# Kernel tuning notes

Hardware: AMD Instinct MI355X
Metric: run time of the kernel (lower is better)

## Reference

```python
import jax, jax.numpy as jnp
import numpy as np

N_TOKENS = 4096
HIDDEN = 1024
FFN = 2048
N_EXPERTS = 8
TOP_K = 2


def setup_inputs() -> dict:
    key = jax.random.key(0)
    k1, k2, k3, k4 = jax.random.split(key, 4)
    x = jax.random.normal(k1, (N_TOKENS, HIDDEN), dtype=jnp.float32)
    router_weight = jax.random.normal(k2, (HIDDEN, N_EXPERTS), dtype=jnp.float32)
    # matches torch.randn(...) * 0.02 init scale
    w1 = jax.random.normal(k3, (HIDDEN, FFN * N_EXPERTS), dtype=jnp.float32) * 0.02
    w2 = jax.random.normal(k4, (FFN * N_EXPERTS, HIDDEN), dtype=jnp.float32) * 0.02
    return {"x": x, "router_weight": router_weight, "w1": w1, "w2": w2, "top_k": TOP_K}


def reference(x, router_weight, w1, w2, top_k):
    # x: [N, H]; router_weight: [H, E]; w1: [H, E*F]; w2: [E*F, H]
    N, H = x.shape
    E = router_weight.shape[1]
    F = w1.shape[1] // E

    # --- routing (router in fp32, softmax over experts, top-k probs) ---
    logits = x.astype(jnp.float32) @ router_weight            # [N, E]
    probs = jax.nn.softmax(logits, axis=-1)                   # [N, E]
    topk_probs, topk_idx = jax.lax.top_k(probs, top_k)        # [N, k]

    # --- expert FFN: per-expert gelu(x @ w1_e) @ w2_e ---
    # Dense formulation: compute every expert for every token, then gather the
    # top-k outputs per token. Same math as grouped-GEMM dispatch/combine.
    h = jax.nn.gelu(x @ w1, approximate=False)                # [N, E*F]
    h = h.reshape(N, E, F)
    w2e = w2.reshape(E, F, H)
    y = jnp.einsum('nef,efh->neh', h, w2e)                    # [N, E, H]

    # --- combine: weight selected expert outputs by router probs, sum top-k ---
    sel = jnp.take_along_axis(y, topk_idx[:, :, None], axis=1)   # [N, k, H]
    out = (sel * topk_probs[:, :, None].astype(sel.dtype)).sum(axis=1)  # [N, H]
    return out
```

## Files before the change

### kernel.cpp

```cpp
#include <hip/hip_runtime.h>
#include <hip/hip_bf16.h>
#include <math.h>

#define N_TOK 4096
#define HID   1024
#define FFN   2048
#define NEXP  8
#define WROW  (NEXP*FFN)
#define NSLOT (N_TOK*2)
#define NCHUNK (NSLOT/64)

typedef __attribute__((ext_vector_type(4))) float f32x4;
typedef __attribute__((ext_vector_type(8))) short short8;

__device__ inline unsigned short f2bf(float f) {
  union { float f; unsigned u; } v; v.f = f;
  unsigned r = v.u + 0x7fffu + ((v.u >> 16) & 1u);
  return (unsigned short)(r >> 16);
}
__device__ __forceinline__ float bf2f(unsigned short u) {
  union { unsigned u; float f; } v; v.u = ((unsigned)u) << 16; return v.f;
}

__device__ __forceinline__ float gelu_f(float v) {
  const float u = 1.5957691216057308f * v + 0.07135481627f * (v * v * v);
  return v / (1.f + __expf(-u));
}

__device__ __forceinline__ void gload16(const void* g, void* l) {
  __builtin_amdgcn_global_load_lds((const __attribute__((address_space(1))) void*)g,
                                   (__attribute__((address_space(3))) void*)l, 16, 0, 0);
}


__global__ __launch_bounds__(256) void router_kernel(
    const float* __restrict__ x, const float* __restrict__ rw,
    int* __restrict__ eidx, float* __restrict__ probs,
    unsigned short* __restrict__ xb) {
  __shared__ float rwT[NEXP][HID];
  const int t = threadIdx.x;
  #pragma unroll
  for (int it = 0; it < 8; ++it) {
    const int flat = t * 4 + it * 1024;
    const f32x4 v = *(const f32x4*)&rw[flat];
    #pragma unroll
    for (int j = 0; j < 4; ++j) rwT[(flat + j) & 7][(flat + j) >> 3] = v[j];
  }
  __syncthreads();

  const int w = t >> 6, l = t & 63;
  const int n = blockIdx.x * 4 + w;
  const float* xr = x + (size_t)n * HID;
  float acc[NEXP];
  #pragma unroll
  for (int e = 0; e < NEXP; ++e) acc[e] = 0.f;

  #pragma unroll
  for (int j = 0; j < 4; ++j) {
    const int i = l * 4 + j * 256;
    const f32x4 xv = *(const f32x4*)&xr[i];
    if (xb) {
      ushort4 o;
      o.x = f2bf(xv[0]); o.y = f2bf(xv[1]); o.z = f2bf(xv[2]); o.w = f2bf(xv[3]);
      *(ushort4*)&xb[(size_t)n * HID + i] = o;
    }
    #pragma unroll
    for (int e = 0; e < NEXP; ++e) {
      const f32x4 wv = *(const f32x4*)&rwT[e][i];
      acc[e] += xv[0] * wv[0] + xv[1] * wv[1] + xv[2] * wv[2] + xv[3] * wv[3];
    }
  }
  #pragma unroll
  for (int e = 0; e < NEXP; ++e) {
    float s = acc[e];
    #pragma unroll
    for (int off = 32; off; off >>= 1) s += __shfl_xor(s, off);
    acc[e] = s;
  }
  if (l == 0) {
    float m = acc[0];
    #pragma unroll
    for (int e = 1; e < NEXP; ++e) m = fmaxf(m, acc[e]);
    float p[NEXP]; float den = 0.f;
    #pragma unroll
    for (int e = 0; e < NEXP; ++e) { p[e] = expf(acc[e] - m); den += p[e]; }
    const float inv = 1.f / den;
    int e1 = 0; float b1 = -1.f;
    #pragma unroll
    for (int e = 0; e < NEXP; ++e) if (p[e] > b1) { b1 = p[e]; e1 = e; }
    int e2 = 0; float b2 = -1.f;
    #pragma unroll
    for (int e = 0; e < NEXP; ++e) if (e != e1 && p[e] > b2) { b2 = p[e]; e2 = e; }
    eidx[n * 2 + 0] = e1; eidx[n * 2 + 1] = e2;
    probs[n * 2 + 0] = b1 * inv; probs[n * 2 + 1] = b2 * inv;
  }
}

__global__ __launch_bounds__(256) void dispatch_kernel(
    const int* __restrict__ eidx, const float* __restrict__ probs,
    int* __restrict__ counts, int* __restrict__ offs,
    int* __restrict__ rowtok, float* __restrict__ rowprob,
    int* __restrict__ tokslot) {
  __shared__ int chunkbase[NCHUNK][NEXP];
  __shared__ int tot[NEXP], off_s[NEXP];
  const int t = threadIdx.x;
  const int w = t >> 6, l = t & 63;

  for (int c = w; c < NCHUNK; c += 4) {
    const int e = eidx[c * 64 + l];
    #pragma unroll
    for (int xp = 0; xp < NEXP; ++xp) {
      const unsigned long long m = __ballot(e == xp);
      if (l == xp) chunkbase[c][xp] = __popcll(m);
    }
  }
  __syncthreads();

  if (t < NEXP) {
    int a = 0;
    for (int c = 0; c < NCHUNK; ++c) {
      const int v = chunkbase[c][t];
      chunkbase[c][t] = a;
      a += v;
    }
    tot[t] = a;
  }
  __syncthreads();
  if (t == 0) {
    int a = 0;
    for (int e = 0; e < NEXP; ++e) { off_s[e] = a; offs[e] = a; counts[e] = tot[e]; a += tot[e]; }
  }
  __syncthreads();

  for (int c = w; c < NCHUNK; c += 4) {
    const int s = c * 64 + l;
    const int e = eidx[s];
    unsigned long long mask_e = 0;
    #pragma unroll
    for (int xp = 0; xp < NEXP; ++xp) {
      const unsigned long long m = __ballot(e == xp);
      if (e == xp) mask_e = m;
    }
    const unsigned long long below = mask_e & ((1ull << l) - 1ull);
    const int pos = off_s[e] + chunkbase[c][e] + __popcll(below);
    rowtok[pos]  = s >> 1;
    rowprob[pos] = probs[s];
    tokslot[s]   = pos;
  }
}

__global__ __launch_bounds__(256) void tconv_kernel(
    const float* __restrict__ in, unsigned short* __restrict__ out,
    int R, int C, int RB) {
  __shared__ float tile[64][65];
  const int r0 = blockIdx.y * 64, c0 = blockIdx.x * 64;
  const int t = threadIdx.x;
  const int tr = t >> 4;
  const int tc4 = (t & 15) * 4;
  #pragma unroll
  for (int i = 0; i < 4; ++i) {
    const int r = tr + i * 16;
    const f32x4 v = *(const f32x4*)&in[(size_t)(r0 + r) * C + c0 + tc4];
    tile[r][tc4 + 0] = v[0]; tile[r][tc4 + 1] = v[1];
    tile[r][tc4 + 2] = v[2]; tile[r][tc4 + 3] = v[3];
  }
  __syncthreads();
  const int eb  = r0 / RB;
  const int rm0 = r0 % RB;
  #pragma unroll
  for (int i = 0; i < 4; ++i) {
    const int c = tr + i * 16;
    ushort4 o;
    o.x = f2bf(tile[tc4 + 0][c]); o.y = f2bf(tile[tc4 + 1][c]);
    o.z = f2bf(tile[tc4 + 2][c]); o.w = f2bf(tile[tc4 + 3][c]);
    const size_t oidx = (size_t)eb * C * RB + (size_t)(c0 + c) * RB + rm0 + tc4;
    *(ushort4*)&out[oidx] = o;
  }
}

__global__ __launch_bounds__(256) void gemm1_fast(
    const unsigned short* __restrict__ xb, const unsigned short* __restrict__ w1t,
    const int* __restrict__ rowtok, const int* __restrict__ counts,
    const int* __restrict__ offs, unsigned short* __restrict__ h1) {
  int wg = blockIdx.x;
  wg = (wg & 7) * (8192 / 8) + (wg >> 3);
  const int bx = wg & 15;
  const int by = (wg >> 4) & 63;
  const int e  = wg >> 10;

  const int cnt = counts[e];
  const int m0  = by * 128;
  if (m0 >= cnt) return;
  const int n0  = bx * 128;
  const int seg = offs[e];

  __shared__ alignas(16) unsigned short Al[3][128 * 32];
  __shared__ alignas(16) unsigned short Bl[3][128 * 32];

  const int t  = threadIdx.x;
  const int l  = t & 63;
  const int w  = t >> 6;
  const int wr = w >> 1, wc = w & 1;
  const int lr = l & 15, hi = l >> 4;

  const int rowS = t >> 2;
  const int kc   = (((t & 3) ^ ((t >> 3) & 3)) * 8);
  const int ra0 = m0 + rowS      < cnt ? m0 + rowS      : cnt - 1;
  const int ra1 = m0 + rowS + 64 < cnt ? m0 + rowS + 64 : cnt - 1;
  const unsigned short* aptr0 = xb + (size_t)rowtok[seg + ra0] * HID + kc;
  const unsigned short* aptr1 = xb + (size_t)rowtok[seg + ra1] * HID + kc;
  const unsigned short* bptr0 = w1t + ((size_t)e * FFN + n0 + rowS)      * HID + kc;
  const unsigned short* bptr1 = w1t + ((size_t)e * FFN + n0 + rowS + 64) * HID + kc;
  const int ldst = (t & 192) * 8;
  const int koff = (hi ^ ((lr >> 1) & 3)) * 8;

  f32x4 acc[4][4];
  #pragma unroll
  for (int i = 0; i < 4; ++i)
    #pragma unroll
    for (int j = 0; j < 4; ++j) acc[i][j] = (f32x4){0.f, 0.f, 0.f, 0.f};

  auto STAGE = [&](int b, int k0) {
    gload16(aptr0 + k0, &Al[b][ldst]);
    gload16(aptr1 + k0, &Al[b][ldst + 2048]);
    gload16(bptr0 + k0, &Bl[b][ldst]);
    gload16(bptr1 + k0, &Bl[b][ldst + 2048]);
  };
  auto COMPUTE = [&](int b) {
    short8 af[4], bfr[4];
    #pragma unroll
    for (int mi = 0; mi < 4; ++mi) af[mi]  = *(const short8*)&Al[b][(wr * 64 + mi * 16 + lr) * 32 + koff];
    #pragma unroll
    for (int ni = 0; ni < 4; ++ni) bfr[ni] = *(const short8*)&Bl[b][(wc * 64 + ni * 16 + lr) * 32 + koff];
    __builtin_amdgcn_s_setprio(1);
    #pragma unroll
    for (int mi = 0; mi < 4; ++mi)
      #pragma unroll
      for (int ni = 0; ni < 4; ++ni)
        acc[mi][ni] = __builtin_amdgcn_mfma_f32_16x16x32_bf16(af[mi], bfr[ni], acc[mi][ni], 0, 0, 0);
    __builtin_amdgcn_s_setprio(0);
  };

  const int NT = HID / 32;
  STAGE(0, 0);
  STAGE(1, 32);
  asm volatile("s_waitcnt vmcnt(4)" ::: "memory");
  __builtin_amdgcn_s_barrier();
  __builtin_amdgcn_sched_barrier(0);
  int cur = 0;
  for (int tt = 0; tt < NT; ++tt) {
    if (tt + 2 < NT) {
      int b2 = cur + 2; if (b2 >= 3) b2 -= 3;
      STAGE(b2, (tt + 2) * 32);
    }
    COMPUTE(cur);
    if (tt + 1 < NT) {
      if (tt + 2 < NT) asm volatile("s_waitcnt vmcnt(4)" ::: "memory");
      else             asm volatile("s_waitcnt vmcnt(0)" ::: "memory");
      __builtin_amdgcn_s_barrier();
      __builtin_amdgcn_sched_barrier(0);
    }
    ++cur; if (cur == 3) cur = 0;
  }

  #pragma unroll
  for (int mi = 0; mi < 4; ++mi) {
    #pragma unroll
    for (int r = 0; r < 4; ++r) {
      const int grow = m0 + wr * 64 + mi * 16 + hi * 4 + r;
      if (grow < cnt) {
        const size_t rowoff = (size_t)(seg + grow) * FFN + n0 + wc * 64 + lr;
        #pragma unroll
        for (int ni = 0; ni < 4; ++ni)
          h1[rowoff + ni * 16] = f2bf(gelu_f(acc[mi][ni][r]));
      }
    }
  }
}

template<int KS>
__global__ __launch_bounds__(256) void gemm2_fast(
    const unsigned short* __restrict__ h1, const unsigned short* __restrict__ w2t,
    const int* __restrict__ counts, const int* __restrict__ offs,
    unsigned short* __restrict__ y) {
  constexpr int G = 8 * 64 * 8 * KS;
  int wg = blockIdx.x;
  wg = (wg & 7) * (G / 8) + (wg >> 3);
  const int bx  = wg & 7;
  const int by  = (wg >> 3) & 63;
  const int bzz = wg >> 9;
  const int e   = bzz & 7;
  const int kz  = bzz >> 3;

  const int cnt = counts[e];
  const int m0  = by * 128;
  if (m0 >= cnt) return;
  const int n0  = bx * 128;
  const int seg = offs[e];
  constexpr int KLEN = FFN / KS;
  const int kbase = kz * KLEN;

  __shared__ alignas(16) unsigned short Al[3][128 * 32];
  __shared__ alignas(16) unsigned short Bl[3][128 * 32];

  const int t  = threadIdx.x;
  const int l  = t & 63;
  const int w  = t >> 6;
  const int wr = w >> 1, wc = w & 1;
  const int lr = l & 15, hi = l >> 4;

  const int rowS = t >> 2;
  const int kc   = (((t & 3) ^ ((t >> 3) & 3)) * 8);
  const int ra0 = m0 + rowS      < cnt ? m0 + rowS      : cnt - 1;
  const int ra1 = m0 + rowS + 64 < cnt ? m0 + rowS + 64 : cnt - 1;
  const unsigned short* aptr0 = h1 + (size_t)(seg + ra0) * FFN + kbase + kc;
  const unsigned short* aptr1 = h1 + (size_t)(seg + ra1) * FFN + kbase + kc;
  const unsigned short* bptr0 = w2t + ((size_t)e * HID + n0 + rowS)      * FFN + kbase + kc;
  const unsigned short* bptr1 = w2t + ((size_t)e * HID + n0 + rowS + 64) * FFN + kbase + kc;
  const int ldst = (t & 192) * 8;
  const int koff = (hi ^ ((lr >> 1) & 3)) * 8;

  f32x4 acc[4][4];
  #pragma unroll
  for (int i = 0; i < 4; ++i)
    #pragma unroll
    for (int j = 0; j < 4; ++j) acc[i][j] = (f32x4){0.f, 0.f, 0.f, 0.f};

  auto STAGE = [&](int b, int k0) {
    gload16(aptr0 + k0, &Al[b][ldst]);
    gload16(aptr1 + k0, &Al[b][ldst + 2048]);
    gload16(bptr0 + k0, &Bl[b][ldst]);
    gload16(bptr1 + k0, &Bl[b][ldst + 2048]);
  };
  auto COMPUTE = [&](int b) {
    short8 af[4], bfr[4];
    #pragma unroll
    for (int mi = 0; mi < 4; ++mi) af[mi]  = *(const short8*)&Al[b][(wr * 64 + mi * 16 + lr) * 32 + koff];
    #pragma unroll
    for (int ni = 0; ni < 4; ++ni) bfr[ni] = *(const short8*)&Bl[b][(wc * 64 + ni * 16 + lr) * 32 + koff];
    __builtin_amdgcn_s_setprio(1);
    #pragma unroll
    for (int mi = 0; mi < 4; ++mi)
      #pragma unroll
      for (int ni = 0; ni < 4; ++ni)
        acc[mi][ni] = __builtin_amdgcn_mfma_f32_16x16x32_bf16(af[mi], bfr[ni], acc[mi][ni], 0, 0, 0);
    __builtin_amdgcn_s_setprio(0);
  };

  const int NT = KLEN / 32;
  STAGE(0, 0);
  STAGE(1, 32);
  asm volatile("s_waitcnt vmcnt(4)" ::: "memory");
  __builtin_amdgcn_s_barrier();
  __builtin_amdgcn_sched_barrier(0);
  int cur = 0;
  for (int tt = 0; tt < NT; ++tt) {
    if (tt + 2 < NT) {
      int b2 = cur + 2; if (b2 >= 3) b2 -= 3;
      STAGE(b2, (tt + 2) * 32);
    }
    COMPUTE(cur);
    if (tt + 1 < NT) {
      if (tt + 2 < NT) asm volatile("s_waitcnt vmcnt(4)" ::: "memory");
      else             asm volatile("s_waitcnt vmcnt(0)" ::: "memory");
      __builtin_amdgcn_s_barrier();
      __builtin_amdgcn_sched_barrier(0);
    }
    ++cur; if (cur == 3) cur = 0;
  }

  #pragma unroll
  for (int mi = 0; mi < 4; ++mi) {
    #pragma unroll
    for (int r = 0; r < 4; ++r) {
      const int grow = m0 + wr * 64 + mi * 16 + hi * 4 + r;
      if (grow < cnt) {
        const int slot = seg + grow;
        unsigned short* yrow = y + ((size_t)kz * NSLOT + slot) * HID + n0 + wc * 64 + lr;
        #pragma unroll
        for (int ni = 0; ni < 4; ++ni)
          yrow[ni * 16] = f2bf(acc[mi][ni][r]);
      }
    }
  }
}

template<int KS>
__global__ __launch_bounds__(256) void combine_kernel(
    const unsigned short* __restrict__ y, const int* __restrict__ tokslot,
    const float* __restrict__ probs, float* __restrict__ out) {
  const int n = blockIdx.x;
  const int c = threadIdx.x * 4;
  const int s1 = tokslot[n * 2 + 0], s2 = tokslot[n * 2 + 1];
  const float p1 = probs[n * 2 + 0], p2 = probs[n * 2 + 1];
  float r0 = 0.f, r1 = 0.f, r2 = 0.f, r3 = 0.f;
  #pragma unroll
  for (int kz = 0; kz < KS; ++kz) {
    const ushort4 a = *(const ushort4*)&y[((size_t)kz * NSLOT + s1) * HID + c];
    const ushort4 b = *(const ushort4*)&y[((size_t)kz * NSLOT + s2) * HID + c];
    r0 += p1 * bf2f(a.x) + p2 * bf2f(b.x);
    r1 += p1 * bf2f(a.y) + p2 * bf2f(b.y);
    r2 += p1 * bf2f(a.z) + p2 * bf2f(b.z);
    r3 += p1 * bf2f(a.w) + p2 * bf2f(b.w);
  }
  *(f32x4*)&out[(size_t)n * HID + c] = (f32x4){r0, r1, r2, r3};
}

__global__ __launch_bounds__(256) void gemm2_fast_atomic(
    const unsigned short* __restrict__ h1, const unsigned short* __restrict__ w2t,
    const int* __restrict__ rowtok, const float* __restrict__ rowprob,
    const int* __restrict__ counts, const int* __restrict__ offs,
    float* __restrict__ out) {
  const int e   = blockIdx.z;
  const int cnt = counts[e];
  const int m0  = blockIdx.y * 128;
  if (m0 >= cnt) return;
  const int n0  = blockIdx.x * 128;
  const int seg = offs[e];

  __shared__ alignas(16) unsigned short Al[128 * 32];
  __shared__ alignas(16) unsigned short Bl[128 * 32];

  const int t  = threadIdx.x;
  const int l  = t & 63;
  const int w  = t >> 6;
  const int wr = w >> 1, wc = w & 1;
  const int lr = l & 15, hi = l >> 4;

  const int rowS = t >> 2;
  const int kc   = (((t & 3) ^ ((t >> 3) & 3)) * 8);
  const int ra0 = m0 + rowS      < cnt ? m0 + rowS      : cnt - 1;
  const int ra1 = m0 + rowS + 64 < cnt ? m0 + rowS + 64 : cnt - 1;
  const unsigned short* aptr0 = h1 + (size_t)(seg + ra0) * FFN + kc;
  const unsigned short* aptr1 = h1 + (size_t)(seg + ra1) * FFN + kc;
  const unsigned short* bptr0 = w2t + ((size_t)e * HID + n0 + rowS)      * FFN + kc;
  const unsigned short* bptr1 = w2t + ((size_t)e * HID + n0 + rowS + 64) * FFN + kc;
  unsigned short* const ldsA0 = Al + (t & 192) * 8;
  unsigned short* const ldsB0 = Bl + (t & 192) * 8;
  const int koff = (hi ^ ((lr >> 1) & 3)) * 8;

  f32x4 acc[4][4];
  #pragma unroll
  for (int i = 0; i < 4; ++i)
    #pragma unroll
    for (int j = 0; j < 4; ++j) acc[i][j] = (f32x4){0.f, 0.f, 0.f, 0.f};

  for (int k0 = 0; k0 < FFN; k0 += 32) {
    gload16(aptr0 + k0, ldsA0);
    gload16(aptr1 + k0, ldsA0 + 2048);
    gload16(bptr0 + k0, ldsB0);
    gload16(bptr1 + k0, ldsB0 + 2048);
    __syncthreads();
    short8 af[4], bfr[4];
    #pragma unroll
    for (int mi = 0; mi < 4; ++mi) af[mi]  = *(const short8*)&Al[(wr * 64 + mi * 16 + lr) * 32 + koff];
    #pragma unroll
    for (int ni = 0; ni < 4; ++ni) bfr[ni] = *(const short8*)&Bl[(wc * 64 + ni * 16 + lr) * 32 + koff];
    #pragma unroll
    for (int mi = 0; mi < 4; ++mi)
      #pragma unroll
      for (int ni = 0; ni < 4; ++ni)
        acc[mi][ni] = __builtin_amdgcn_mfma_f32_16x16x32_bf16(af[mi], bfr[ni], acc[mi][ni], 0, 0, 0);
    __syncthreads();
  }

  #pragma unroll
  for (int mi = 0; mi < 4; ++mi) {
    #pragma unroll
    for (int r = 0; r < 4; ++r) {
      const int grow = m0 + wr * 64 + mi * 16 + hi * 4 + r;
      if (grow < cnt) {
        const int slot = seg + grow;
        const int tok  = rowtok[slot];
        const float p  = rowprob[slot];
        #pragma unroll
        for (int ni = 0; ni < 4; ++ni)
          atomicAdd(&out[(size_t)tok * HID + n0 + wc * 64 + ni * 16 + lr], p * acc[mi][ni][r]);
      }
    }
  }
}

__global__ __launch_bounds__(256) void gemm1_old(
    const float* __restrict__ x, const float* __restrict__ w1,
    const int* __restrict__ rowtok, const int* __restrict__ counts,
    const int* __restrict__ offs, unsigned short* __restrict__ h1) {
  const int e   = blockIdx.z;
  const int cnt = counts[e];
  const int m0  = blockIdx.y * 64;
  if (m0 >= cnt) return;
  const int n0  = blockIdx.x * 64;
  const int seg = offs[e];
  __shared__ unsigned short Al[64 * 40];
  __shared__ unsigned short Bl[64 * 40];
  const int t  = threadIdx.x;
  const int l  = t & 63;
  const int wv = t >> 6;
  const int wr = wv >> 1, wc = wv & 1;
  const int am  = t >> 2;
  const int akb = (t & 3) * 8;
  const int amg = m0 + am;
  const bool aval = (amg < cnt);
  const float* aptr = aval ? (x + (size_t)rowtok[seg + amg] * HID + akb) : x;
  const int bn  = t & 63;
  const int bkg = (t >> 6) * 8;
  const float* bptr = w1 + (size_t)e * FFN + n0 + bn;
  f32x4 acc[2][2];
  #pragma unroll
  for (int i = 0; i < 2; ++i)
    #pragma unroll
    for (int j = 0; j < 2; ++j) acc[i][j] = (f32x4){0.f, 0.f, 0.f, 0.f};
  const int kreg = (l >> 4) * 8;
  const int lr   = l & 15;
  for (int k0 = 0; k0 < HID; k0 += 32) {
    short8 av = (short8){0,0,0,0,0,0,0,0};
    if (aval) {
      const f32x4 v0 = *(const f32x4*)(aptr + k0);
      const f32x4 v1 = *(const f32x4*)(aptr + k0 + 4);
      #pragma unroll
      for (int j = 0; j < 4; ++j) { av[j] = (short)f2bf(v0[j]); av[4 + j] = (short)f2bf(v1[j]); }
    }
    *(short8*)&Al[am * 40 + akb] = av;
    short8 bv;
    #pragma unroll
    for (int j = 0; j < 8; ++j) bv[j] = (short)f2bf(bptr[(size_t)(k0 + bkg + j) * WROW]);
    *(short8*)&Bl[bn * 40 + bkg] = bv;
    __syncthreads();
    short8 af[2], bfr[2];
    #pragma unroll
    for (int mi = 0; mi < 2; ++mi) af[mi]  = *(const short8*)&Al[(wr * 32 + mi * 16 + lr) * 40 + kreg];
    #pragma unroll
    for (int ni = 0; ni < 2; ++ni) bfr[ni] = *(const short8*)&Bl[(wc * 32 + ni * 16 + lr) * 40 + kreg];
    #pragma unroll
    for (int mi = 0; mi < 2; ++mi)
      #pragma unroll
      for (int ni = 0; ni < 2; ++ni)
        acc[mi][ni] = __builtin_amdgcn_mfma_f32_16x16x32_bf16(af[mi], bfr[ni], acc[mi][ni], 0, 0, 0);
    __syncthreads();
  }
  const int kq = l >> 4;
  #pragma unroll
  for (int mi = 0; mi < 2; ++mi) {
    #pragma unroll
    for (int r = 0; r < 4; ++r) {
      const int grow = m0 + wr * 32 + mi * 16 + kq * 4 + r;
      if (grow < cnt) {
        #pragma unroll
        for (int ni = 0; ni < 2; ++ni) {
          const float v = acc[mi][ni][r];
          const float g = 0.5f * v * (1.0f + erff(v * 0.70710678118654752f));
          h1[(size_t)(seg + grow) * FFN + n0 + wc * 32 + ni * 16 + lr] = f2bf(g);
        }
      }
    }
  }
}

__global__ __launch_bounds__(256) void gemm2_old(
    const unsigned short* __restrict__ h1, const float* __restrict__ w2,
    const int* __restrict__ rowtok, const float* __restrict__ rowprob,
    const int* __restrict__ counts, const int* __restrict__ offs,
    float* __restrict__ out) {
  const int e   = blockIdx.z;
  const int cnt = counts[e];
  const int m0  = blockIdx.y * 64;
  if (m0 >= cnt) return;
  const int n0  = blockIdx.x * 64;
  const int seg = offs[e];
  __shared__ unsigned short Al[64 * 40];
  __shared__ unsigned short Bl[64 * 40];
  const int t  = threadIdx.x;
  const int l  = t & 63;
  const int wv = t >> 6;
  const int wr = wv >> 1, wc = wv & 1;
  const int am  = t >> 2;
  const int akb = (t & 3) * 8;
  const int amg = m0 + am;
  const bool aval = (amg < cnt);
  const unsigned short* aptr = aval ? (h1 + (size_t)(seg + amg) * FFN + akb) : h1;
  const int bn  = t & 63;
  const int bkg = (t >> 6) * 8;
  const float* bptr = w2 + (size_t)e * FFN * HID + n0 + bn;
  f32x4 acc[2][2];
  #pragma unroll
  for (int i = 0; i < 2; ++i)
    #pragma unroll
    for (int j = 0; j < 2; ++j) acc[i][j] = (f32x4){0.f, 0.f, 0.f, 0.f};
  const int kreg = (l >> 4) * 8;
  const int lr   = l & 15;
  for (int k0 = 0; k0 < FFN; k0 += 32) {
    short8 av = (short8){0,0,0,0,0,0,0,0};
    if (aval) av = *(const short8*)(aptr + k0);
    *(short8*)&Al[am * 40 + akb] = av;
    short8 bv;
    #pragma unroll
    for (int j = 0; j < 8; ++j) bv[j] = (short)f2bf(bptr[(size_t)(k0 + bkg + j) * HID]);
    *(short8*)&Bl[bn * 40 + bkg] = bv;
    __syncthreads();
    short8 af[2], bfr[2];
    #pragma unroll
    for (int mi = 0; mi < 2; ++mi) af[mi]  = *(const short8*)&Al[(wr * 32 + mi * 16 + lr) * 40 + kreg];
    #pragma unroll
    for (int ni = 0; ni < 2; ++ni) bfr[ni] = *(const short8*)&Bl[(wc * 32 + ni * 16 + lr) * 40 + kreg];
    #pragma unroll
    for (int mi = 0; mi < 2; ++mi)
      #pragma unroll
      for (int ni = 0; ni < 2; ++ni)
        acc[mi][ni] = __builtin_amdgcn_mfma_f32_16x16x32_bf16(af[mi], bfr[ni], acc[mi][ni], 0, 0, 0);
    __syncthreads();
  }
  const int kq = l >> 4;
  #pragma unroll
  for (int mi = 0; mi < 2; ++mi) {
    #pragma unroll
    for (int r = 0; r < 4; ++r) {
      const int grow = m0 + wr * 32 + mi * 16 + kq * 4 + r;
      if (grow < cnt) {
        const int slot = seg + grow;
        const int tok  = rowtok[slot];
        const float p  = rowprob[slot];
        #pragma unroll
        for (int ni = 0; ni < 2; ++ni)
          atomicAdd(&out[(size_t)tok * HID + n0 + wc * 32 + ni * 16 + lr], p * acc[mi][ni][r]);
      }
    }
  }
}

extern "C" void kernel_launch(void* const* d_in, const int* in_sizes, int n_in,
                              void* d_out, int out_size, void* d_ws, size_t ws_size,
                              hipStream_t stream) {
  const float* x  = (const float*)d_in[0];
  const float* rw = (const float*)d_in[1];
  const float* w1 = (const float*)d_in[2];
  const float* w2 = (const float*)d_in[3];
  float* out = (float*)d_out;

  int*   counts  = (int*)d_ws;
  int*   offs    = counts + 8;
  int*   tokslot = counts + 16;
  int*   eidx    = tokslot + NSLOT;
  float* probs   = (float*)(eidx + NSLOT);
  int*   rowtok  = (int*)(probs + NSLOT);
  float* rowprob = (float*)(rowtok + NSLOT);
  unsigned short* h1 = (unsigned short*)(rowprob + NSLOT);
  unsigned short* xb = h1 + (size_t)NSLOT * FFN;
  unsigned short* wt = xb + (size_t)N_TOK * HID;
  unsigned short* y  = wt + (size_t)WROW * HID;

  const size_t need_base = (size_t)((char*)y - (char*)d_ws);
  const size_t need_y1   = need_base + (size_t)NSLOT * HID * 2;
  const size_t need_y2   = need_base + (size_t)2 * NSLOT * HID * 2;
  const bool fast = (ws_size >= need_base);

  router_kernel<<<N_TOK / 4, 256, 0, stream>>>(x, rw, eidx, probs, fast ? xb : nullptr);
  dispatch_kernel<<<1, 256, 0, stream>>>(eidx, probs, counts, offs, rowtok, rowprob, tokslot);

  if (fast) {
    tconv_kernel<<<dim3(WROW / 64, HID / 64), 256, 0, stream>>>(w1, wt, HID, WROW, HID);
    gemm1_fast<<<16 * 64 * 8, 256, 0, stream>>>(xb, wt, rowtok, counts, offs, h1);
    tconv_kernel<<<dim3(HID / 64, WROW / 64), 256, 0, stream>>>(w2, wt, WROW, HID, FFN);
    if (ws_size >= need_y2) {
      gemm2_fast<2><<<8 * 64 * 8 * 2, 256, 0, stream>>>(h1, wt, counts, offs, y);
      combine_kernel<2><<<N_TOK, 256, 0, stream>>>(y, tokslot, probs, out);
    } else if (ws_size >= need_y1) {
      gemm2_fast<1><<<8 * 64 * 8, 256, 0, stream>>>(h1, wt, counts, offs, y);
      combine_kernel<1><<<N_TOK, 256, 0, stream>>>(y, tokslot, probs, out);
    } else {
      hipMemsetAsync(d_out, 0, (size_t)out_size * sizeof(float), stream);
      gemm2_fast_atomic<<<dim3(HID / 128, NSLOT / 128, NEXP), 256, 0, stream>>>(h1, wt, rowtok, rowprob, counts, offs, out);
    }
  } else {
    hipMemsetAsync(d_out, 0, (size_t)out_size * sizeof(float), stream);
    gemm1_old<<<dim3(FFN / 64, NSLOT / 64, NEXP), 256, 0, stream>>>(x, w1, rowtok, counts, offs, h1);
    gemm2_old<<<dim3(HID / 64, NSLOT / 64, NEXP), 256, 0, stream>>>(h1, w2, rowtok, rowprob, counts, offs, out);
  }
}
```

Baseline: 207.4 us.

## Shrink GEMM grids to persistent M-loop and merge weight conversions into one kernel

The grouped GEMMs now launch a fixed grid with nine M-tile slots per expert. Each block loops over M tiles with a stride of nine, instead of launching 64 M tiles per expert, most of which exit early. The two weight transpose-and-convert passes are merged into a single launch writing to separate buffers, which needs extra workspace. This removes early-exit blocks and a launch, but an expert with many tokens can leave some blocks running long serial loops.

```diff
diff --git a/kernel.cpp b/kernel.cpp
--- a/kernel.cpp
+++ b/kernel.cpp
@@ -178,19 +178,56 @@
   }
 }
 
+__global__ __launch_bounds__(256) void tconv_both_kernel(
+    const float* __restrict__ w1, const float* __restrict__ w2,
+    unsigned short* __restrict__ w1t, unsigned short* __restrict__ w2t) {
+  __shared__ float tile[64][65];
+  int b = blockIdx.x;
+  const float* in; unsigned short* out; int C, RB, r0, c0;
+  if (b < 4096) {
+    in = w1; out = w1t; C = WROW; RB = HID;
+    c0 = (b & 255) * 64; r0 = (b >> 8) * 64;
+  } else {
+    b -= 4096;
+    in = w2; out = w2t; C = HID; RB = FFN;
+    c0 = (b & 15) * 64; r0 = (b >> 4) * 64;
+  }
+  const int t = threadIdx.x;
+  const int tr = t >> 4;
+  const int tc4 = (t & 15) * 4;
+  #pragma unroll
+  for (int i = 0; i < 4; ++i) {
+    const int r = tr + i * 16;
+    const f32x4 v = *(const f32x4*)&in[(size_t)(r0 + r) * C + c0 + tc4];
+    tile[r][tc4 + 0] = v[0]; tile[r][tc4 + 1] = v[1];
+    tile[r][tc4 + 2] = v[2]; tile[r][tc4 + 3] = v[3];
+  }
+  __syncthreads();
+  const int eb  = r0 / RB;
+  const int rm0 = r0 % RB;
+  #pragma unroll
+  for (int i = 0; i < 4; ++i) {
+    const int c = tr + i * 16;
+    ushort4 o;
+    o.x = f2bf(tile[tc4 + 0][c]); o.y = f2bf(tile[tc4 + 1][c]);
+    o.z = f2bf(tile[tc4 + 2][c]); o.w = f2bf(tile[tc4 + 3][c]);
+    const size_t oidx = (size_t)eb * C * RB + (size_t)(c0 + c) * RB + rm0 + tc4;
+    *(ushort4*)&out[oidx] = o;
+  }
+}
+
 __global__ __launch_bounds__(256) void gemm1_fast(
     const unsigned short* __restrict__ xb, const unsigned short* __restrict__ w1t,
     const int* __restrict__ rowtok, const int* __restrict__ counts,
     const int* __restrict__ offs, unsigned short* __restrict__ h1) {
   int wg = blockIdx.x;
-  wg = (wg & 7) * (8192 / 8) + (wg >> 3);
+  wg = (wg & 7) * (1152 / 8) + (wg >> 3);
   const int bx = wg & 15;
-  const int by = (wg >> 4) & 63;
-  const int e  = wg >> 10;
+  const int rest = wg >> 4;
+  const int by = rest % 9;
+  const int e  = rest / 9;
 
   const int cnt = counts[e];
-  const int m0  = by * 128;
-  if (m0 >= cnt) return;
   const int n0  = bx * 128;
   const int seg = offs[e];
 
@@ -205,74 +242,81 @@
 
   const int rowS = t >> 2;
   const int kc   = (((t & 3) ^ ((t >> 3) & 3)) * 8);
-  const int ra0 = m0 + rowS      < cnt ? m0 + rowS      : cnt - 1;
-  const int ra1 = m0 + rowS + 64 < cnt ? m0 + rowS + 64 : cnt - 1;
-  const unsigned short* aptr0 = xb + (size_t)rowtok[seg + ra0] * HID + kc;
-  const unsigned short* aptr1 = xb + (size_t)rowtok[seg + ra1] * HID + kc;
-  const unsigned short* bptr0 = w1t + ((size_t)e * FFN + n0 + rowS)      * HID + kc;
-  const unsigned short* bptr1 = w1t + ((size_t)e * FFN + n0 + rowS + 64) * HID + kc;
+  const unsigned short* bptr0 = w1t + ((size_t)e * FFN + n0 + rowS) * HID + kc;
+  const unsigned short* bptr1 = bptr0 + (size_t)64 * HID;
   const int ldst = (t & 192) * 8;
   const int koff = (hi ^ ((lr >> 1) & 3)) * 8;
-
-  f32x4 acc[4][4];
-  #pragma unroll
-  for (int i = 0; i < 4; ++i)
-    #pragma unroll
-    for (int j = 0; j < 4; ++j) acc[i][j] = (f32x4){0.f, 0.f, 0.f, 0.f};
-
-  auto STAGE = [&](int b, int k0) {
-    gload16(aptr0 + k0, &Al[b][ldst]);
-    gload16(aptr1 + k0, &Al[b][ldst + 2048]);
-    gload16(bptr0 + k0, &Bl[b][ldst]);
-    gload16(bptr1 + k0, &Bl[b][ldst + 2048]);
-  };
-  auto COMPUTE = [&](int b) {
-    short8 af[4], bfr[4];
-    #pragma unroll
-    for (int mi = 0; mi < 4; ++mi) af[mi]  = *(const short8*)&Al[b][(wr * 64 + mi * 16 + lr) * 32 + koff];
-    #pragma unroll
-    for (int ni = 0; ni < 4; ++ni) bfr[ni] = *(const short8*)&Bl[b][(wc * 64 + ni * 16 + lr) * 32 + koff];
-    __builtin_amdgcn_s_setprio(1);
-    #pragma unroll
-    for (int mi = 0; mi < 4; ++mi)
-      #pragma unroll
-      for (int ni = 0; ni < 4; ++ni)
-        acc[mi][ni] = __builtin_amdgcn_mfma_f32_16x16x32_bf16(af[mi], bfr[ni], acc[mi][ni], 0, 0, 0);
-    __builtin_amdgcn_s_setprio(0);
-  };
-
   const int NT = HID / 32;
-  STAGE(0, 0);
-  STAGE(1, 32);
-  asm volatile("s_waitcnt vmcnt(4)" ::: "memory");
-  __builtin_amdgcn_s_barrier();
-  __builtin_amdgcn_sched_barrier(0);
-  int cur = 0;
-  for (int tt = 0; tt < NT; ++tt) {
-    if (tt + 2 < NT) {
-      int b2 = cur + 2; if (b2 >= 3) b2 -= 3;
-      STAGE(b2, (tt + 2) * 32);
-    }
-    COMPUTE(cur);
-    if (tt + 1 < NT) {
-      if (tt + 2 < NT) asm volatile("s_waitcnt vmcnt(4)" ::: "memory");
-      else             asm volatile("s_waitcnt vmcnt(0)" ::: "memory");
-      __builtin_amdgcn_s_barrier();
-      __builtin_amdgcn_sched_barrier(0);
-    }
-    ++cur; if (cur == 3) cur = 0;
-  }
-
-  #pragma unroll
-  for (int mi = 0; mi < 4; ++mi) {
-    #pragma unroll
-    for (int r = 0; r < 4; ++r) {
-      const int grow = m0 + wr * 64 + mi * 16 + hi * 4 + r;
-      if (grow < cnt) {
-        const size_t rowoff = (size_t)(seg + grow) * FFN + n0 + wc * 64 + lr;
+
+  bool firstm = true;
+  for (int m0 = by * 128; m0 < cnt; m0 += 9 * 128) {
+    if (!firstm) __syncthreads();
+    firstm = false;
+
+    const int ra0 = m0 + rowS      < cnt ? m0 + rowS      : cnt - 1;
+    const int ra1 = m0 + rowS + 64 < cnt ? m0 + rowS + 64 : cnt - 1;
+    const unsigned short* aptr0 = xb + (size_t)rowtok[seg + ra0] * HID + kc;
+    const unsigned short* aptr1 = xb + (size_t)rowtok[seg + ra1] * HID + kc;
+
+    f32x4 acc[4][4];
+    #pragma unroll
+    for (int i = 0; i < 4; ++i)
+      #pragma unroll
+      for (int j = 0; j < 4; ++j) acc[i][j] = (f32x4){0.f, 0.f, 0.f, 0.f};
+
+    auto STAGE = [&](int b, int k0) {
+      gload16(aptr0 + k0, &Al[b][ldst]);
+      gload16(aptr1 + k0, &Al[b][ldst + 2048]);
+      gload16(bptr0 + k0, &Bl[b][ldst]);
+      gload16(bptr1 + k0, &Bl[b][ldst + 2048]);
+    };
+    auto COMPUTE = [&](int b) {
+      short8 af[4], bfr[4];
+      #pragma unroll
+      for (int mi = 0; mi < 4; ++mi) af[mi]  = *(const short8*)&Al[b][(wr * 64 + mi * 16 + lr) * 32 + koff];
+      #pragma unroll
+      for (int ni = 0; ni < 4; ++ni) bfr[ni] = *(const short8*)&Bl[b][(wc * 64 + ni * 16 + lr) * 32 + koff];
+      __builtin_amdgcn_s_setprio(1);
+      #pragma unroll
+      for (int mi = 0; mi < 4; ++mi)
         #pragma unroll
         for (int ni = 0; ni < 4; ++ni)
-          h1[rowoff + ni * 16] = f2bf(gelu_f(acc[mi][ni][r]));
+          acc[mi][ni] = __builtin_amdgcn_mfma_f32_16x16x32_bf16(af[mi], bfr[ni], acc[mi][ni], 0, 0, 0);
+      __builtin_amdgcn_s_setprio(0);
+    };
+
+    STAGE(0, 0);
+    STAGE(1, 32);
+    asm volatile("s_waitcnt vmcnt(4)" ::: "memory");
+    __builtin_amdgcn_s_barrier();
+    __builtin_amdgcn_sched_barrier(0);
+    int cur = 0;
+    for (int tt = 0; tt < NT; ++tt) {
+      if (tt + 2 < NT) {
+        int b2 = cur + 2; if (b2 >= 3) b2 -= 3;
+        STAGE(b2, (tt + 2) * 32);
+      }
+      COMPUTE(cur);
+      if (tt + 1 < NT) {
+        if (tt + 2 < NT) asm volatile("s_waitcnt vmcnt(4)" ::: "memory");
+        else             asm volatile("s_waitcnt vmcnt(0)" ::: "memory");
+        __builtin_amdgcn_s_barrier();
+        __builtin_amdgcn_sched_barrier(0);
+      }
+      ++cur; if (cur == 3) cur = 0;
+    }
+
+    #pragma unroll
+    for (int mi = 0; mi < 4; ++mi) {
+      #pragma unroll
+      for (int r = 0; r < 4; ++r) {
+        const int grow = m0 + wr * 64 + mi * 16 + hi * 4 + r;
+        if (grow < cnt) {
+          const size_t rowoff = (size_t)(seg + grow) * FFN + n0 + wc * 64 + lr;
+          #pragma unroll
+          for (int ni = 0; ni < 4; ++ni)
+            h1[rowoff + ni * 16] = f2bf(gelu_f(acc[mi][ni][r]));
+        }
       }
     }
   }
@@ -283,18 +327,17 @@
     const unsigned short* __restrict__ h1, const unsigned short* __restrict__ w2t,
     const int* __restrict__ counts, const int* __restrict__ offs,
     unsigned short* __restrict__ y) {
-  constexpr int G = 8 * 64 * 8 * KS;
+  constexpr int G = 576 * KS;
   int wg = blockIdx.x;
   wg = (wg & 7) * (G / 8) + (wg >> 3);
   const int bx  = wg & 7;
-  const int by  = (wg >> 3) & 63;
-  const int bzz = wg >> 9;
-  const int e   = bzz & 7;
-  const int kz  = bzz >> 3;
+  int rest = wg >> 3;
+  const int by  = rest % 9;
+  rest /= 9;
+  const int e   = rest & 7;
+  const int kz  = rest >> 3;
 
   const int cnt = counts[e];
-  const int m0  = by * 128;
-  if (m0 >= cnt) return;
   const int n0  = bx * 128;
   const int seg = offs[e];
   constexpr int KLEN = FFN / KS;
@@ -311,75 +354,82 @@
 
   const int rowS = t >> 2;
   const int kc   = (((t & 3) ^ ((t >> 3) & 3)) * 8);
-  const int ra0 = m0 + rowS      < cnt ? m0 + rowS      : cnt - 1;
-  const int ra1 = m0 + rowS + 64 < cnt ? m0 + rowS + 64 : cnt - 1;
-  const unsigned short* aptr0 = h1 + (size_t)(seg + ra0) * FFN + kbase + kc;
-  const unsigned short* aptr1 = h1 + (size_t)(seg + ra1) * FFN + kbase + kc;
-  const unsigned short* bptr0 = w2t + ((size_t)e * HID + n0 + rowS)      * FFN + kbase + kc;
-  const unsigned short* bptr1 = w2t + ((size_t)e * HID + n0 + rowS + 64) * FFN + kbase + kc;
+  const unsigned short* bptr0 = w2t + ((size_t)e * HID + n0 + rowS) * FFN + kbase + kc;
+  const unsigned short* bptr1 = bptr0 + (size_t)64 * FFN;
   const int ldst = (t & 192) * 8;
   const int koff = (hi ^ ((lr >> 1) & 3)) * 8;
-
-  f32x4 acc[4][4];
-  #pragma unroll
-  for (int i = 0; i < 4; ++i)
-    #pragma unroll
-    for (int j = 0; j < 4; ++j) acc[i][j] = (f32x4){0.f, 0.f, 0.f, 0.f};
-
-  auto STAGE = [&](int b, int k0) {
-    gload16(aptr0 + k0, &Al[b][ldst]);
-    gload16(aptr1 + k0, &Al[b][ldst + 2048]);
-    gload16(bptr0 + k0, &Bl[b][ldst]);
-    gload16(bptr1 + k0, &Bl[b][ldst + 2048]);
-  };
-  auto COMPUTE = [&](int b) {
-    short8 af[4], bfr[4];
-    #pragma unroll
-    for (int mi = 0; mi < 4; ++mi) af[mi]  = *(const short8*)&Al[b][(wr * 64 + mi * 16 + lr) * 32 + koff];
-    #pragma unroll
-    for (int ni = 0; ni < 4; ++ni) bfr[ni] = *(const short8*)&Bl[b][(wc * 64 + ni * 16 + lr) * 32 + koff];
-    __builtin_amdgcn_s_setprio(1);
-    #pragma unroll
-    for (int mi = 0; mi < 4; ++mi)
-      #pragma unroll
-      for (int ni = 0; ni < 4; ++ni)
-        acc[mi][ni] = __builtin_amdgcn_mfma_f32_16x16x32_bf16(af[mi], bfr[ni], acc[mi][ni], 0, 0, 0);
-    __builtin_amdgcn_s_setprio(0);
-  };
-
   const int NT = KLEN / 32;
-  STAGE(0, 0);
-  STAGE(1, 32);
-  asm volatile("s_waitcnt vmcnt(4)" ::: "memory");
-  __builtin_amdgcn_s_barrier();
-  __builtin_amdgcn_sched_barrier(0);
-  int cur = 0;
-  for (int tt = 0; tt < NT; ++tt) {
-    if (tt + 2 < NT) {
-      int b2 = cur + 2; if (b2 >= 3) b2 -= 3;
-      STAGE(b2, (tt + 2) * 32);
-    }
-    COMPUTE(cur);
-    if (tt + 1 < NT) {
-      if (tt + 2 < NT) asm volatile("s_waitcnt vmcnt(4)" ::: "memory");
-      else             asm volatile("s_waitcnt vmcnt(0)" ::: "memory");
-      __builtin_amdgcn_s_barrier();
-      __builtin_amdgcn_sched_barrier(0);
-    }
-    ++cur; if (cur == 3) cur = 0;
-  }
-
-  #pragma unroll
-  for (int mi = 0; mi < 4; ++mi) {
-    #pragma unroll
-    for (int r = 0; r < 4; ++r) {
-      const int grow = m0 + wr * 64 + mi * 16 + hi * 4 + r;
-      if (grow < cnt) {
-        const int slot = seg + grow;
-        unsigned short* yrow = y + ((size_t)kz * NSLOT + slot) * HID + n0 + wc * 64 + lr;
+
+  bool firstm = true;
+  for (int m0 = by * 128; m0 < cnt; m0 += 9 * 128) {
+    if (!firstm) __syncthreads();
+    firstm = false;
+
+    const int ra0 = m0 + rowS      < cnt ? m0 + rowS      : cnt - 1;
+    const int ra1 = m0 + rowS + 64 < cnt ? m0 + rowS + 64 : cnt - 1;
+    const unsigned short* aptr0 = h1 + (size_t)(seg + ra0) * FFN + kbase + kc;
+    const unsigned short* aptr1 = h1 + (size_t)(seg + ra1) * FFN + kbase + kc;
+
+    f32x4 acc[4][4];
+    #pragma unroll
+    for (int i = 0; i < 4; ++i)
+      #pragma unroll
+      for (int j = 0; j < 4; ++j) acc[i][j] = (f32x4){0.f, 0.f, 0.f, 0.f};
+
+    auto STAGE = [&](int b, int k0) {
+      gload16(aptr0 + k0, &Al[b][ldst]);
+      gload16(aptr1 + k0, &Al[b][ldst + 2048]);
+      gload16(bptr0 + k0, &Bl[b][ldst]);
+      gload16(bptr1 + k0, &Bl[b][ldst + 2048]);
+    };
+    auto COMPUTE = [&](int b) {
+      short8 af[4], bfr[4];
+      #pragma unroll
+      for (int mi = 0; mi < 4; ++mi) af[mi]  = *(const short8*)&Al[b][(wr * 64 + mi * 16 + lr) * 32 + koff];
+      #pragma unroll
+      for (int ni = 0; ni < 4; ++ni) bfr[ni] = *(const short8*)&Bl[b][(wc * 64 + ni * 16 + lr) * 32 + koff];
+      __builtin_amdgcn_s_setprio(1);
+      #pragma unroll
+      for (int mi = 0; mi < 4; ++mi)
         #pragma unroll
         for (int ni = 0; ni < 4; ++ni)
-          yrow[ni * 16] = f2bf(acc[mi][ni][r]);
+          acc[mi][ni] = __builtin_amdgcn_mfma_f32_16x16x32_bf16(af[mi], bfr[ni], acc[mi][ni], 0, 0, 0);
+      __builtin_amdgcn_s_setprio(0);
+    };
+
+    STAGE(0, 0);
+    STAGE(1, 32);
+    asm volatile("s_waitcnt vmcnt(4)" ::: "memory");
+    __builtin_amdgcn_s_barrier();
+    __builtin_amdgcn_sched_barrier(0);
+    int cur = 0;
+    for (int tt = 0; tt < NT; ++tt) {
+      if (tt + 2 < NT) {
+        int b2 = cur + 2; if (b2 >= 3) b2 -= 3;
+        STAGE(b2, (tt + 2) * 32);
+      }
+      COMPUTE(cur);
+      if (tt + 1 < NT) {
+        if (tt + 2 < NT) asm volatile("s_waitcnt vmcnt(4)" ::: "memory");
+        else             asm volatile("s_waitcnt vmcnt(0)" ::: "memory");
+        __builtin_amdgcn_s_barrier();
+        __builtin_amdgcn_sched_barrier(0);
+      }
+      ++cur; if (cur == 3) cur = 0;
+    }
+
+    #pragma unroll
+    for (int mi = 0; mi < 4; ++mi) {
+      #pragma unroll
+      for (int r = 0; r < 4; ++r) {
+        const int grow = m0 + wr * 64 + mi * 16 + hi * 4 + r;
+        if (grow < cnt) {
+          const int slot = seg + grow;
+          unsigned short* yrow = y + ((size_t)kz * NSLOT + slot) * HID + n0 + wc * 64 + lr;
+          #pragma unroll
+          for (int ni = 0; ni < 4; ++ni)
+            yrow[ni * 16] = f2bf(acc[mi][ni][r]);
+        }
       }
     }
   }
@@ -643,29 +693,37 @@
   float* probs   = (float*)(eidx + NSLOT);
   int*   rowtok  = (int*)(probs + NSLOT);
   float* rowprob = (float*)(rowtok + NSLOT);
-  unsigned short* h1 = (unsigned short*)(rowprob + NSLOT);
-  unsigned short* xb = h1 + (size_t)NSLOT * FFN;
-  unsigned short* wt = xb + (size_t)N_TOK * HID;
-  unsigned short* y  = wt + (size_t)WROW * HID;
-
-  const size_t need_base = (size_t)((char*)y - (char*)d_ws);
-  const size_t need_y1   = need_base + (size_t)NSLOT * HID * 2;
-  const size_t need_y2   = need_base + (size_t)2 * NSLOT * HID * 2;
+  unsigned short* h1  = (unsigned short*)(rowprob + NSLOT);
+  unsigned short* xb  = h1 + (size_t)NSLOT * FFN;
+  unsigned short* wt  = xb + (size_t)N_TOK * HID;
+  unsigned short* wt2 = wt + (size_t)WROW * HID;
+  unsigned short* ymg = wt2 + (size_t)WROW * HID;
+
+  const size_t need_base   = (size_t)((char*)wt2 - (char*)d_ws);
+  const size_t need_seq_y1 = need_base + (size_t)NSLOT * HID * 2;
+  const size_t need_seq_y2 = need_base + (size_t)2 * NSLOT * HID * 2;
+  const size_t need_mrg_y2 = need_base + (size_t)WROW * HID * 2
+                             + (size_t)2 * NSLOT * HID * 2;
   const bool fast = (ws_size >= need_base);
 
   router_kernel<<<N_TOK / 4, 256, 0, stream>>>(x, rw, eidx, probs, fast ? xb : nullptr);
   dispatch_kernel<<<1, 256, 0, stream>>>(eidx, probs, counts, offs, rowtok, rowprob, tokslot);
 
-  if (fast) {
+  if (fast && ws_size >= need_mrg_y2) {
+    tconv_both_kernel<<<8192, 256, 0, stream>>>(w1, w2, wt, wt2);
+    gemm1_fast<<<1152, 256, 0, stream>>>(xb, wt, rowtok, counts, offs, h1);
+    gemm2_fast<2><<<1152, 256, 0, stream>>>(h1, wt2, counts, offs, ymg);
+    combine_kernel<2><<<N_TOK, 256, 0, stream>>>(ymg, tokslot, probs, out);
+  } else if (fast) {
     tconv_kernel<<<dim3(WROW / 64, HID / 64), 256, 0, stream>>>(w1, wt, HID, WROW, HID);
-    gemm1_fast<<<16 * 64 * 8, 256, 0, stream>>>(xb, wt, rowtok, counts, offs, h1);
+    gemm1_fast<<<1152, 256, 0, stream>>>(xb, wt, rowtok, counts, offs, h1);
     tconv_kernel<<<dim3(HID / 64, WROW / 64), 256, 0, stream>>>(w2, wt, WROW, HID, FFN);
-    if (ws_size >= need_y2) {
-      gemm2_fast<2><<<8 * 64 * 8 * 2, 256, 0, stream>>>(h1, wt, counts, offs, y);
-      combine_kernel<2><<<N_TOK, 256, 0, stream>>>(y, tokslot, probs, out);
-    } else if (ws_size >= need_y1) {
-      gemm2_fast<1><<<8 * 64 * 8, 256, 0, stream>>>(h1, wt, counts, offs, y);
-      combine_kernel<1><<<N_TOK, 256, 0, stream>>>(y, tokslot, probs, out);
+    if (ws_size >= need_seq_y2) {
+      gemm2_fast<2><<<1152, 256, 0, stream>>>(h1, wt, counts, offs, wt2);
+      combine_kernel<2><<<N_TOK, 256, 0, stream>>>(wt2, tokslot, probs, out);
+    } else if (ws_size >= need_seq_y1) {
+      gemm2_fast<1><<<576, 256, 0, stream>>>(h1, wt, counts, offs, wt2);
+      combine_kernel<1><<<N_TOK, 256, 0, stream>>>(wt2, tokslot, probs, out);
     } else {
       hipMemsetAsync(d_out, 0, (size_t)out_size * sizeof(float), stream);
       gemm2_fast_atomic<<<dim3(HID / 128, NSLOT / 128, NEXP), 256, 0, stream>>>(h1, wt, rowtok, rowprob, counts, offs, out);
```

Result: no change. 206.8 us (-0.3%).
